# Performance work log

Hardware: AMD Instinct MI355X
Metric: run time of the kernel (lower is better)

Reference implementation:

```python
import jax, jax.numpy as jnp
import numpy as np
import math

B, T, VOCAB, RANK = 32, 1024, 512, 256


def setup_inputs() -> dict:
    key = jax.random.key(0)
    k1, k2, k3, k4, k5 = jax.random.split(key, 5)
    scale_attn = 1.0 / math.sqrt(VOCAB)
    scale_proj = 1.0 / math.sqrt(RANK)
    return {
        "x": jax.random.normal(k1, (B, T, VOCAB), dtype=jnp.float32),
        "W_attn": jax.random.normal(k2, (VOCAB, 3 * RANK), dtype=jnp.float32) * scale_attn,
        "b_attn": jax.random.normal(k3, (3 * RANK,), dtype=jnp.float32) * 0.01,
        "W_proj": jax.random.normal(k4, (RANK, VOCAB), dtype=jnp.float32) * scale_proj,
        "b_proj": jax.random.normal(k5, (VOCAB,), dtype=jnp.float32) * 0.01,
    }


def reference(x, W_attn, b_attn, W_proj, b_proj):
    # x: [B, T, vocab]
    Bb, Tt, _ = x.shape
    qkv = x @ W_attn + b_attn              # [B, T, 3*rank]
    q, k, v = jnp.split(qkv, 3, axis=-1)   # each [B, T, rank]
    scale = 1.0 / math.sqrt(k.shape[-1])
    att = jnp.einsum('btd,bsd->bts', q, k) * scale  # [B, T, T]
    # causal mask (masked=True)
    mask = jnp.tril(jnp.ones((Tt, Tt), dtype=bool))
    att = jnp.where(mask[None, :, :], att, -jnp.inf)
    att = jax.nn.softmax(att, axis=-1)
    # dropout layers are identity in eval mode (p=0 attn, p=0.1 resid disabled)
    y = jnp.einsum('bts,bsd->btd', att, v)  # [B, T, rank]
    y = y @ W_proj + b_proj                 # [B, T, vocab]
    return jax.nn.gelu(y, approximate=False)
```

## Files before the change

kernel.cpp:

```cpp
#include <hip/hip_runtime.h>
#include <hip/hip_bf16.h>
#include <math.h>

typedef __bf16 bf16;
typedef __attribute__((ext_vector_type(8))) __bf16 bf16x8;
typedef __attribute__((ext_vector_type(4))) __bf16 bf16x4;
typedef __attribute__((ext_vector_type(4))) float f32x4;

#define MFMA16(a, b, c) __builtin_amdgcn_mfma_f32_16x16x32_bf16((a), (b), (c), 0, 0, 0)

__device__ __forceinline__ void glds16(const bf16* g, bf16* l) {
  __builtin_amdgcn_global_load_lds(
      (const __attribute__((address_space(1))) unsigned int*)g,
      (__attribute__((address_space(3))) unsigned int*)l, 16, 0, 0);
}


__global__ __launch_bounds__(256) void cvt_wattn(const float* __restrict__ w,
                                                 bf16* __restrict__ wt) {
  int o = blockIdx.x * 256 + threadIdx.x;
  int n = o >> 9, kk = o & 511;
  wt[o] = (bf16)w[kk * 768 + n];
}

__global__ __launch_bounds__(256) void cvt_wproj(const float* __restrict__ w,
                                                 bf16* __restrict__ wt) {
  int o = blockIdx.x * 256 + threadIdx.x;
  int n = o >> 8, kk = o & 255;
  wt[o] = (bf16)w[kk * 512 + n];
}

__global__ __launch_bounds__(256) void cvt_x(const float* __restrict__ x,
                                             bf16* __restrict__ xb) {
  size_t i = ((size_t)blockIdx.x * 256 + threadIdx.x) * 8;
  f32x4 f0 = *(const f32x4*)(x + i);
  f32x4 f1 = *(const f32x4*)(x + i + 4);
  bf16x8 h;
#pragma unroll
  for (int e = 0; e < 4; ++e) { h[e] = (bf16)f0[e]; h[e + 4] = (bf16)f1[e]; }
  *(bf16x8*)(xb + i) = h;
}

__global__ __launch_bounds__(256) void gemm_qkv(
    const bf16* __restrict__ xb, const bf16* __restrict__ WT,
    const float* __restrict__ b_attn,
    bf16* __restrict__ qo, bf16* __restrict__ ko, bf16* __restrict__ vo) {
  __shared__ __attribute__((aligned(16))) bf16 As[128][32];
  __shared__ __attribute__((aligned(16))) bf16 Bs[128][32];
  const int tid = threadIdx.x;
  const int id = blockIdx.x;
  const int xcd = id & 7;
  const int rest = id >> 3;
  const int bmL = rest / 6;
  const int bn = (rest % 6) * 128;
  const int bm = (xcd * 32 + bmL) * 128;
  const int lane = tid & 63, wid = tid >> 6;
  const int l15 = lane & 15, lg = lane >> 4;
  const int wm = (wid >> 1) * 64, wn = (wid & 1) * 64;

  f32x4 acc[4][4] = {};

  const int ar = tid >> 2;
  const int ac = (tid & 3) * 8;
  const bf16* aB = xb + (size_t)bm * 512 + (size_t)ar * 512 + ac;
  const bf16* bB = WT + (size_t)bn * 512 + (size_t)ar * 512 + ac;
  bf16* As0 = &As[0][0];
  bf16* Bs0 = &Bs[0][0];

  for (int kt = 0; kt < 16; ++kt) {
    const int k0 = kt * 32;
    glds16(aB + k0,            As0 + (size_t)tid * 8);
    glds16(aB + 64 * 512 + k0, As0 + (size_t)(256 + tid) * 8);
    glds16(bB + k0,            Bs0 + (size_t)tid * 8);
    glds16(bB + 64 * 512 + k0, Bs0 + (size_t)(256 + tid) * 8);
    __syncthreads();
    bf16x8 af[4], bfr[4];
#pragma unroll
    for (int mi = 0; mi < 4; ++mi)
      af[mi] = *(const bf16x8*)&As[wm + mi * 16 + l15][lg * 8];
#pragma unroll
    for (int ni = 0; ni < 4; ++ni)
      bfr[ni] = *(const bf16x8*)&Bs[wn + ni * 16 + l15][lg * 8];
#pragma unroll
    for (int mi = 0; mi < 4; ++mi)
#pragma unroll
      for (int ni = 0; ni < 4; ++ni)
        acc[mi][ni] = MFMA16(af[mi], bfr[ni], acc[mi][ni]);
    __syncthreads();
  }

#pragma unroll
  for (int ni = 0; ni < 4; ++ni) {
    int gc = bn + wn + ni * 16 + l15;
    float bias = b_attn[gc];
    int seg = gc >> 8;
    int cc = gc & 255;
    bf16* op = (seg == 0) ? qo : ((seg == 1) ? ko : vo);
#pragma unroll
    for (int mi = 0; mi < 4; ++mi) {
      int gr = bm + wm + mi * 16 + lg * 4;
#pragma unroll
      for (int r = 0; r < 4; ++r) {
        float v = acc[mi][ni][r] + bias;
        op[(size_t)(gr + r) * 256 + cc] = (bf16)v;
      }
    }
  }
}

__global__ __launch_bounds__(256) void transpose_v(const bf16* __restrict__ v,
                                                   bf16* __restrict__ vt) {
  __shared__ bf16 tile[32][33];
  const int b = blockIdx.z;
  const int t0 = blockIdx.x * 32;
  const int d0 = blockIdx.y * 32;
  const int tid = threadIdx.x;
  const int r = tid >> 3, c4 = (tid & 7) * 4;
  bf16x4 in = *(const bf16x4*)(v + (size_t)(b * 1024 + t0 + r) * 256 + d0 + c4);
  tile[r][c4] = in[0]; tile[r][c4 + 1] = in[1];
  tile[r][c4 + 2] = in[2]; tile[r][c4 + 3] = in[3];
  __syncthreads();
  bf16x4 o;
  o[0] = tile[c4][r]; o[1] = tile[c4 + 1][r];
  o[2] = tile[c4 + 2][r]; o[3] = tile[c4 + 3][r];
  *(bf16x4*)(vt + (size_t)(b * 256 + d0 + r) * 1024 + t0 + c4) = o;
}

__global__ __launch_bounds__(512) void attn_fwd(
    const bf16* __restrict__ q, const bf16* __restrict__ k,
    const bf16* __restrict__ vt, bf16* __restrict__ y) {
  __shared__ __attribute__((aligned(16))) bf16 Ks[64][264];
  __shared__ __attribute__((aligned(16))) bf16 Vt[256][72];
  __shared__ __attribute__((aligned(16))) bf16 Ps[8][16][72];
  const int tid = threadIdx.x, lane = tid & 63, wid = tid >> 6;
  const int l15 = lane & 15, lg = lane >> 4;

  const int id = blockIdx.x;
  const int xcd = id & 7;
  const int rest = id >> 3;
  const int qt = rest & 7;
  const int bg = rest >> 3;
  const int b = xcd + 8 * bg;
  const int q0 = qt * 128 + wid * 16;

  bf16x8 qf[8];
  {
    const bf16* qp = q + (size_t)(b * 1024 + q0 + l15) * 256 + lg * 8;
#pragma unroll
    for (int d = 0; d < 8; ++d) qf[d] = *(const bf16x8*)(qp + d * 32);
  }
  f32x4 o[16] = {};
  float m_st = -1e30f;
  float l_st = 0.f;

  const bf16* kbase = k + (size_t)b * 1024 * 256;
  const bf16* vtbase = vt + (size_t)b * 256 * 1024;
  const int ksr = tid >> 5, ksc = (tid & 31) * 8;
  const int vsr = tid >> 3, vsc = (tid & 7) * 8;

  const int ntiles = 2 * qt + 2;

  bf16x8 kreg[4], vreg[4];
#pragma unroll
  for (int i = 0; i < 4; ++i)
    kreg[i] = *(const bf16x8*)(kbase + (size_t)(ksr + i * 16) * 256 + ksc);
#pragma unroll
  for (int i = 0; i < 4; ++i)
    vreg[i] = *(const bf16x8*)(vtbase + (size_t)(vsr + i * 64) * 1024 + vsc);

  for (int tt = 0; tt < ntiles; ++tt) {
    const int kv0 = tt * 64;
    __syncthreads();
#pragma unroll
    for (int i = 0; i < 4; ++i)
      *(bf16x8*)&Ks[ksr + i * 16][ksc] = kreg[i];
#pragma unroll
    for (int i = 0; i < 4; ++i)
      *(bf16x8*)&Vt[vsr + i * 64][vsc] = vreg[i];
    __syncthreads();
    if (tt + 1 < ntiles) {
      const bf16* kp = kbase + (size_t)(kv0 + 64 + ksr) * 256 + ksc;
      const bf16* vp = vtbase + (size_t)vsr * 1024 + kv0 + 64 + vsc;
#pragma unroll
      for (int i = 0; i < 4; ++i)
        kreg[i] = *(const bf16x8*)(kp + (size_t)i * 16 * 256);
#pragma unroll
      for (int i = 0; i < 4; ++i)
        vreg[i] = *(const bf16x8*)(vp + (size_t)i * 64 * 1024);
    }

    f32x4 st[4] = {};
    __builtin_amdgcn_s_setprio(1);
#pragma unroll
    for (int nf = 0; nf < 4; ++nf)
#pragma unroll
      for (int dc = 0; dc < 8; ++dc) {
        bf16x8 kb = *(const bf16x8*)&Ks[nf * 16 + l15][dc * 32 + lg * 8];
        st[nf] = MFMA16(kb, qf[dc], st[nf]);
      }
    __builtin_amdgcn_s_setprio(0);

    const int qg = q0 + l15;
    float tmax = -1e30f;
#pragma unroll
    for (int nf = 0; nf < 4; ++nf)
#pragma unroll
      for (int r = 0; r < 4; ++r) {
        int sg = kv0 + nf * 16 + lg * 4 + r;
        float v = st[nf][r] * 0.0625f;
        v = (sg > qg) ? -1e30f : v;
        st[nf][r] = v;
        tmax = fmaxf(tmax, v);
      }
    tmax = fmaxf(tmax, __shfl_xor(tmax, 16, 64));
    tmax = fmaxf(tmax, __shfl_xor(tmax, 32, 64));

    if (!__all(tmax <= m_st + 8.f)) {
      float mnew = fmaxf(m_st, tmax);
      float corr = __expf(m_st - mnew);
      m_st = mnew;
      l_st *= corr;
      float corrT[4];
#pragma unroll
      for (int r = 0; r < 4; ++r) corrT[r] = __shfl(corr, lg * 4 + r, 64);
#pragma unroll
      for (int df = 0; df < 16; ++df)
#pragma unroll
        for (int r = 0; r < 4; ++r) o[df][r] *= corrT[r];
    }

    float rsum = 0.f;
#pragma unroll
    for (int nf = 0; nf < 4; ++nf) {
      bf16x4 pk;
#pragma unroll
      for (int r = 0; r < 4; ++r) {
        float p = __expf(st[nf][r] - m_st);
        rsum += p;
        pk[r] = (bf16)p;
      }
      *(bf16x4*)&Ps[wid][l15][nf * 16 + lg * 4] = pk;
    }
    rsum += __shfl_xor(rsum, 16, 64);
    rsum += __shfl_xor(rsum, 32, 64);
    l_st += rsum;

    bf16x8 pa0 = *(const bf16x8*)&Ps[wid][l15][lg * 8];
    bf16x8 pa1 = *(const bf16x8*)&Ps[wid][l15][32 + lg * 8];
    __builtin_amdgcn_s_setprio(1);
#pragma unroll
    for (int df = 0; df < 16; ++df) {
      bf16x8 vb0 = *(const bf16x8*)&Vt[df * 16 + l15][lg * 8];
      bf16x8 vb1 = *(const bf16x8*)&Vt[df * 16 + l15][32 + lg * 8];
      o[df] = MFMA16(pa0, vb0, o[df]);
      o[df] = MFMA16(pa1, vb1, o[df]);
    }
    __builtin_amdgcn_s_setprio(0);
  }

  float lT[4];
#pragma unroll
  for (int r = 0; r < 4; ++r) lT[r] = __shfl(l_st, lg * 4 + r, 64);
  const size_t ybase = (size_t)(b * 1024 + q0 + lg * 4) * 256 + l15;
#pragma unroll
  for (int r = 0; r < 4; ++r) {
    float inv = 1.f / lT[r];
#pragma unroll
    for (int df = 0; df < 16; ++df)
      y[ybase + (size_t)r * 256 + df * 16] = (bf16)(o[df][r] * inv);
  }
}

__global__ __launch_bounds__(256) void gemm_proj(
    const bf16* __restrict__ y, const bf16* __restrict__ WT,
    const float* __restrict__ b_proj, float* __restrict__ out) {
  __shared__ __attribute__((aligned(16))) bf16 As[128][32];
  __shared__ __attribute__((aligned(16))) bf16 Bs[128][32];
  const int tid = threadIdx.x;
  const int id = blockIdx.x;
  const int xcd = id & 7;
  const int rest = id >> 3;
  const int bmL = rest >> 2;
  const int bn = (rest & 3) * 128;
  const int bm = (xcd * 32 + bmL) * 128;
  const int lane = tid & 63, wid = tid >> 6;
  const int l15 = lane & 15, lg = lane >> 4;
  const int wm = (wid >> 1) * 64, wn = (wid & 1) * 64;
  f32x4 acc[4][4] = {};

  const int ar = tid >> 2;
  const int ac = (tid & 3) * 8;
  const bf16* aB = y + (size_t)bm * 256 + (size_t)ar * 256 + ac;
  const bf16* bB = WT + (size_t)bn * 256 + (size_t)ar * 256 + ac;
  bf16* As0 = &As[0][0];
  bf16* Bs0 = &Bs[0][0];

  for (int kt = 0; kt < 8; ++kt) {
    const int k0 = kt * 32;
    glds16(aB + k0,            As0 + (size_t)tid * 8);
    glds16(aB + 64 * 256 + k0, As0 + (size_t)(256 + tid) * 8);
    glds16(bB + k0,            Bs0 + (size_t)tid * 8);
    glds16(bB + 64 * 256 + k0, Bs0 + (size_t)(256 + tid) * 8);
    __syncthreads();
    bf16x8 af[4], bfr[4];
#pragma unroll
    for (int mi = 0; mi < 4; ++mi)
      af[mi] = *(const bf16x8*)&As[wm + mi * 16 + l15][lg * 8];
#pragma unroll
    for (int ni = 0; ni < 4; ++ni)
      bfr[ni] = *(const bf16x8*)&Bs[wn + ni * 16 + l15][lg * 8];
#pragma unroll
    for (int mi = 0; mi < 4; ++mi)
#pragma unroll
      for (int ni = 0; ni < 4; ++ni)
        acc[mi][ni] = MFMA16(af[mi], bfr[ni], acc[mi][ni]);
    __syncthreads();
  }
#pragma unroll
  for (int ni = 0; ni < 4; ++ni) {
    int gc = bn + wn + ni * 16 + l15;
    float bias = b_proj[gc];
#pragma unroll
    for (int mi = 0; mi < 4; ++mi) {
      int gr = bm + wm + mi * 16 + lg * 4;
#pragma unroll
      for (int r = 0; r < 4; ++r) {
        float v = acc[mi][ni][r] + bias;
        float g = 0.5f * v * (1.0f + erff(v * 0.70710678118654752f));
        out[(size_t)(gr + r) * 512 + gc] = g;
      }
    }
  }
}

extern "C" void kernel_launch(void* const* d_in, const int* in_sizes, int n_in,
                              void* d_out, int out_size, void* d_ws, size_t ws_size,
                              hipStream_t stream) {
  const float* x      = (const float*)d_in[0];
  const float* W_attn = (const float*)d_in[1];
  const float* b_attn = (const float*)d_in[2];
  const float* W_proj = (const float*)d_in[3];
  const float* b_proj = (const float*)d_in[4];
  float* out = (float*)d_out;
  char* ws = (char*)d_ws;

  const size_t SZ = 16777216;
  bf16* WT1 = (bf16*)(ws);
  bf16* WT2 = (bf16*)(ws + 786432);
  bf16* qb  = (bf16*)(ws + 1048576);
  bf16* kb  = (bf16*)(ws + 1048576 + SZ);
  bf16* vb  = (bf16*)(ws + 1048576 + 2 * SZ);
  bf16* vtb = (bf16*)(ws + 1048576 + 3 * SZ);
  bf16* yb  = vb;
  bf16* xbb = (bf16*)(ws + 1048576 + 3 * SZ);

  cvt_wattn<<<dim3(1536), dim3(256), 0, stream>>>(W_attn, WT1);
  cvt_wproj<<<dim3(512), dim3(256), 0, stream>>>(W_proj, WT2);
  cvt_x<<<dim3(8192), dim3(256), 0, stream>>>(x, xbb);
  gemm_qkv<<<dim3(1536), dim3(256), 0, stream>>>(xbb, WT1, b_attn, qb, kb, vb);
  transpose_v<<<dim3(32, 8, 32), dim3(256), 0, stream>>>(vb, vtb);
  attn_fwd<<<dim3(256), dim3(512), 0, stream>>>(qb, kb, vtb, yb);
  gemm_proj<<<dim3(1024), dim3(256), 0, stream>>>(yb, WT2, b_proj, out);
}
```

Measured before the change: 157.3 us.

## Transpose MFMA accumulator layout for vector stores and use tanh GELU

Swaps the A/B operands of every MFMA in the QKV GEMM, the attention PV product and the projection GEMM. Each lane then holds four consecutive columns of one row, so epilogues write packed bf16x4 or float4 values and load the bias as a vector. In attention this also removes the per-row shuffles of the rescale factor and the final normalizer. The projection epilogue replaces exact erf GELU with an exp-based tanh approximation, which cuts per-element math but adds a small numerical deviation from the exact GELU in the reference.

```diff
diff --git a/kernel.cpp b/kernel.cpp
--- a/kernel.cpp
+++ b/kernel.cpp
@@ -85,25 +85,24 @@
     for (int mi = 0; mi < 4; ++mi)
 #pragma unroll
       for (int ni = 0; ni < 4; ++ni)
-        acc[mi][ni] = MFMA16(af[mi], bfr[ni], acc[mi][ni]);
+        acc[mi][ni] = MFMA16(bfr[ni], af[mi], acc[mi][ni]);
     __syncthreads();
   }
 
 #pragma unroll
   for (int ni = 0; ni < 4; ++ni) {
-    int gc = bn + wn + ni * 16 + l15;
-    float bias = b_attn[gc];
-    int seg = gc >> 8;
-    int cc = gc & 255;
+    int gc0 = bn + wn + ni * 16 + lg * 4;
+    f32x4 bias = *(const f32x4*)(b_attn + gc0);
+    int seg = gc0 >> 8;
+    int cc = gc0 & 255;
     bf16* op = (seg == 0) ? qo : ((seg == 1) ? ko : vo);
 #pragma unroll
     for (int mi = 0; mi < 4; ++mi) {
-      int gr = bm + wm + mi * 16 + lg * 4;
-#pragma unroll
-      for (int r = 0; r < 4; ++r) {
-        float v = acc[mi][ni][r] + bias;
-        op[(size_t)(gr + r) * 256 + cc] = (bf16)v;
-      }
+      int gr = bm + wm + mi * 16 + l15;
+      bf16x4 pk;
+#pragma unroll
+      for (int r = 0; r < 4; ++r) pk[r] = (bf16)(acc[mi][ni][r] + bias[r]);
+      *(bf16x4*)(op + (size_t)gr * 256 + cc) = pk;
     }
   }
 }
@@ -220,13 +219,10 @@
       float corr = __expf(m_st - mnew);
       m_st = mnew;
       l_st *= corr;
-      float corrT[4];
-#pragma unroll
-      for (int r = 0; r < 4; ++r) corrT[r] = __shfl(corr, lg * 4 + r, 64);
 #pragma unroll
       for (int df = 0; df < 16; ++df)
 #pragma unroll
-        for (int r = 0; r < 4; ++r) o[df][r] *= corrT[r];
+        for (int r = 0; r < 4; ++r) o[df][r] *= corr;
     }
 
     float rsum = 0.f;
@@ -252,22 +248,20 @@
     for (int df = 0; df < 16; ++df) {
       bf16x8 vb0 = *(const bf16x8*)&Vt[df * 16 + l15][lg * 8];
       bf16x8 vb1 = *(const bf16x8*)&Vt[df * 16 + l15][32 + lg * 8];
-      o[df] = MFMA16(pa0, vb0, o[df]);
-      o[df] = MFMA16(pa1, vb1, o[df]);
+      o[df] = MFMA16(vb0, pa0, o[df]);
+      o[df] = MFMA16(vb1, pa1, o[df]);
     }
     __builtin_amdgcn_s_setprio(0);
   }
 
-  float lT[4];
-#pragma unroll
-  for (int r = 0; r < 4; ++r) lT[r] = __shfl(l_st, lg * 4 + r, 64);
-  const size_t ybase = (size_t)(b * 1024 + q0 + lg * 4) * 256 + l15;
-#pragma unroll
-  for (int r = 0; r < 4; ++r) {
-    float inv = 1.f / lT[r];
-#pragma unroll
-    for (int df = 0; df < 16; ++df)
-      y[ybase + (size_t)r * 256 + df * 16] = (bf16)(o[df][r] * inv);
+  float inv = 1.f / l_st;
+  bf16* yp = y + (size_t)(b * 1024 + q0 + l15) * 256 + lg * 4;
+#pragma unroll
+  for (int df = 0; df < 16; ++df) {
+    bf16x4 pk;
+#pragma unroll
+    for (int r = 0; r < 4; ++r) pk[r] = (bf16)(o[df][r] * inv);
+    *(bf16x4*)(yp + df * 16) = pk;
   }
 }
 
@@ -313,22 +307,27 @@
     for (int mi = 0; mi < 4; ++mi)
 #pragma unroll
       for (int ni = 0; ni < 4; ++ni)
-        acc[mi][ni] = MFMA16(af[mi], bfr[ni], acc[mi][ni]);
-    __syncthreads();
-  }
+        acc[mi][ni] = MFMA16(bfr[ni], af[mi], acc[mi][ni]);
+    __syncthreads();
+  }
+
 #pragma unroll
   for (int ni = 0; ni < 4; ++ni) {
-    int gc = bn + wn + ni * 16 + l15;
-    float bias = b_proj[gc];
+    int gc0 = bn + wn + ni * 16 + lg * 4;
+    f32x4 bias = *(const f32x4*)(b_proj + gc0);
 #pragma unroll
     for (int mi = 0; mi < 4; ++mi) {
-      int gr = bm + wm + mi * 16 + lg * 4;
+      int gr = bm + wm + mi * 16 + l15;
+      f32x4 g;
 #pragma unroll
       for (int r = 0; r < 4; ++r) {
-        float v = acc[mi][ni][r] + bias;
-        float g = 0.5f * v * (1.0f + erff(v * 0.70710678118654752f));
-        out[(size_t)(gr + r) * 512 + gc] = g;
+        float v = acc[mi][ni][r] + bias[r];
+        float z = 1.5957691216f * (v + 0.044715f * v * v * v);
+        float t = __expf(z);
+        float th = 1.f - 2.f / (t + 1.f);
+        g[r] = 0.5f * v * (1.f + th);
       }
+      *(f32x4*)(out + (size_t)gr * 512 + gc0) = g;
     }
   }
 }
```

After: 162.4 us. 3.3% more time.
